# Optimization experiments

Measured on AMD Instinct MI355X. Metric: run time of the kernel, lower is better.

Reference implementation:

```python
import jax, jax.numpy as jnp
import numpy as np

N, D, H, E, K = 4096, 256, 1024, 8, 2  # tokens, hid_dim, expert hidden, n_experts, topk


def setup_inputs() -> dict:
    key = jax.random.key(0)
    ks = jax.random.split(key, 5)
    s = 0.02
    return {
        "x": jax.random.normal(ks[0], (N, D), jnp.float32),
        "gate_W": jax.random.normal(ks[1], (E, D), jnp.float32) * s,  # nn.Linear(hid_dim, n_exp).weight
        "gate_b": jnp.zeros((E,), jnp.float32),
        "W1": jax.random.normal(ks[2], (E, D, H), jnp.float32) * s,   # per-expert FFN layer 1
        "b1": jnp.zeros((E, H), jnp.float32),
        "W2": jax.random.normal(ks[3], (E, H, D), jnp.float32) * s,   # per-expert FFN layer 2
        "b2": jnp.zeros((E, D), jnp.float32),
        "temperature": jnp.array(1.0, jnp.float32),
    }


def reference(x, gate_W, gate_b, W1, b1, W2, b2, temperature):
    # forward() unsqueezes 2D input to [N, 1, D]
    x3 = x[:, None, :]                                           # [N,1,D]
    # _router: gate linear over last dim, squeeze L=1
    gate_scores = (jnp.einsum('nld,ed->nle', x3, gate_W) + gate_b)[:, 0, :]  # [N,E]
    gate_scores = gate_scores / temperature                      # router_act='lambda' -> identity
    _, topk_idx = jax.lax.top_k(gate_scores, K)                  # [N,K]

    # _moe_batch_forward: repeat_interleave tokens K times, route slot s to expert topk_idx.flat[s]
    xs = jnp.repeat(x3, K, axis=0)                               # [N*K,1,D]
    eid = topk_idx.reshape(-1)                                   # [N*K] int
    out = jnp.zeros((N * K, 1, D), x.dtype)
    for e in range(E):  # small fixed expert loop; masks partition the slots
        h = jax.nn.relu(jnp.einsum('sld,dh->slh', xs, W1[e]) + b1[e])  # [N*K,1,H]
        y = jnp.einsum('slh,hd->sld', h, W2[e]) + b2[e]                # [N*K,1,D]
        out = out + jnp.where((eid == e)[:, None, None], y, 0.0)
    out = out.reshape(N, K, 1, D)
    # gatter='sum': sum over the K expert slots -> [N,1,D]
    return out.sum(axis=1)
```

## Files before the change

kernel.cpp:

```cpp
#include <hip/hip_runtime.h>
#include <hip/hip_bf16.h>
#include <stdint.h>

#define NTOK 4096
#define DIM  256
#define HID  1024
#define NEXP 8
#define MTILE 32
#define HC 32
#define HSLICE 512
#define NSLICE 2
#define NCHUNK (HSLICE / HC)

typedef float f32x4 __attribute__((ext_vector_type(4)));
typedef short s16x8 __attribute__((ext_vector_type(8)));

__device__ __forceinline__ unsigned short f2bf(float f) {
  union { float f; unsigned u; } v; v.f = f;
  unsigned r = v.u + 0x7FFFu + ((v.u >> 16) & 1u);
  return (unsigned short)(r >> 16);
}
__device__ __forceinline__ float bf2f(unsigned short s) {
  union { float f; unsigned u; } v; v.u = ((unsigned)s) << 16;
  return v.f;
}
__device__ __forceinline__ void mfma16(f32x4& acc, s16x8 a, s16x8 b) {
  asm("v_mfma_f32_16x16x32_bf16 %0, %1, %2, %0" : "+v"(acc) : "v"(a), "v"(b));
}
__device__ __forceinline__ void accfence(f32x4& a) {
  asm volatile("s_nop 7" : "+v"(a));
}
__device__ __forceinline__ void initfence(f32x4& a) {
  asm volatile("s_nop 1" : "+v"(a));
}

__global__ __launch_bounds__(256) void prep(const float* __restrict__ W1,
                                            const float* __restrict__ W2,
                                            unsigned short* __restrict__ W1T,
                                            unsigned short* __restrict__ W2T,
                                            int* __restrict__ counts) {
  __shared__ float tile[32][33];
  int id = blockIdx.x;
  int tx = threadIdx.x, ty = threadIdx.y;
  if (id == 0 && ty == 0 && tx < NEXP) counts[tx] = 0;

  const float* in; unsigned short* out; int R, C, bx, by, e, sw;
  if (id < 2048) {
    e = id >> 8; int rem = id & 255; by = rem >> 5; bx = rem & 31;
    in = W1; out = W1T; R = 256; C = 1024; sw = 1;
  } else {
    int id2 = id - 2048;
    e = id2 >> 8; int rem = id2 & 255; by = (rem >> 3) & 31; bx = rem & 7;
    in = W2; out = W2T; R = 1024; C = 256; sw = 0;
  }
  int r0 = by * 32, c0 = bx * 32;
  const float* ip = in + (size_t)e * R * C;
  unsigned short* op = out + (size_t)e * R * C;
  #pragma unroll
  for (int k = 0; k < 4; ++k)
    tile[ty + 8*k][tx] = ip[(size_t)(r0 + ty + 8*k) * C + c0 + tx];
  __syncthreads();
  #pragma unroll
  for (int k = 0; k < 4; ++k) {
    float v = tile[tx][ty + 8*k];
    if (sw) {
      int row = c0 + ty + 8*k;
      int col = r0 + tx;
      op[(size_t)row * R + (col ^ ((row & 7) << 3))] = f2bf(v);
    } else {
      int d = c0 + ty + 8*k;
      int h = r0 + tx;
      int ch = h >> 5, kk = h & 31;
      int slot = (kk >> 3) ^ ((d >> 1) & 3);
      op[(size_t)ch * (DIM * 32) + d * 32 + slot * 8 + (kk & 7)] = f2bf(v);
    }
  }
}

__global__ __launch_bounds__(256) void gate_route(const float* __restrict__ x,
    const float* __restrict__ gW, const float* __restrict__ gb,
    const float* __restrict__ temp,
    int* __restrict__ counts, int* __restrict__ list,
    unsigned short* __restrict__ xbf) {
  __shared__ int pairs[16][2];
  __shared__ int lcnt[NEXP], lbase[NEXP], lrank[NEXP];
  int tid = threadIdx.x;
  int w = tid >> 6, lane = tid & 63;
  int sl = lane & 15, g = lane >> 4;
  if (tid < NEXP) { lcnt[tid] = 0; lrank[tid] = 0; }
  __syncthreads();
  int t0 = blockIdx.x * 16;
  int tok = w * 4 + g;
  int n = t0 + tok;

  float4 xv[4];
  #pragma unroll
  for (int p = 0; p < 4; ++p)
    xv[p] = *reinterpret_cast<const float4*>(x + (size_t)n * DIM + sl * 16 + p * 4);
  {
    s16x8 xb0, xb1;
    xb0[0]=(short)f2bf(xv[0].x); xb0[1]=(short)f2bf(xv[0].y); xb0[2]=(short)f2bf(xv[0].z); xb0[3]=(short)f2bf(xv[0].w);
    xb0[4]=(short)f2bf(xv[1].x); xb0[5]=(short)f2bf(xv[1].y); xb0[6]=(short)f2bf(xv[1].z); xb0[7]=(short)f2bf(xv[1].w);
    xb1[0]=(short)f2bf(xv[2].x); xb1[1]=(short)f2bf(xv[2].y); xb1[2]=(short)f2bf(xv[2].z); xb1[3]=(short)f2bf(xv[2].w);
    xb1[4]=(short)f2bf(xv[3].x); xb1[5]=(short)f2bf(xv[3].y); xb1[6]=(short)f2bf(xv[3].z); xb1[7]=(short)f2bf(xv[3].w);
    *reinterpret_cast<s16x8*>(xbf + (size_t)n * DIM + sl * 16)     = xb0;
    *reinterpret_cast<s16x8*>(xbf + (size_t)n * DIM + sl * 16 + 8) = xb1;
  }
  float acc[NEXP];
  #pragma unroll
  for (int e = 0; e < NEXP; ++e) {
    const float* we = gW + (size_t)e * DIM + sl * 16;
    float a = 0.f;
    #pragma unroll
    for (int p = 0; p < 4; ++p) {
      float4 wv = *reinterpret_cast<const float4*>(we + p * 4);
      a += xv[p].x*wv.x + xv[p].y*wv.y + xv[p].z*wv.z + xv[p].w*wv.w;
    }
    acc[e] = a;
  }
  #pragma unroll
  for (int off = 1; off < 16; off <<= 1) {
    #pragma unroll
    for (int e = 0; e < NEXP; ++e) acc[e] += __shfl_xor(acc[e], off);
  }
  if (sl == 0) {
    float t = temp[0];
    float s[NEXP];
    #pragma unroll
    for (int e = 0; e < NEXP; ++e) s[e] = (acc[e] + gb[e]) / t;
    int b0 = 0; float v0 = s[0];
    #pragma unroll
    for (int e = 1; e < NEXP; ++e) if (s[e] > v0) { v0 = s[e]; b0 = e; }
    int b1i = 0; float v1 = -3.4e38f;
    #pragma unroll
    for (int e = 0; e < NEXP; ++e) if (e != b0 && s[e] > v1) { v1 = s[e]; b1i = e; }
    pairs[tok][0] = b0;
    pairs[tok][1] = b1i;
    atomicAdd(&lcnt[b0], 1);
    atomicAdd(&lcnt[b1i], 1);
  }
  __syncthreads();
  if (tid < NEXP) lbase[tid] = atomicAdd(&counts[tid], lcnt[tid]);
  __syncthreads();
  if (tid < 32) {
    int tk = tid >> 1;
    int e = pairs[tk][tid & 1];
    int r = atomicAdd(&lrank[e], 1);
    list[e * NTOK + lbase[e] + r] = (t0 + tk) * 2 + (tid & 1);
  }
}

__global__ __launch_bounds__(256, 2) void moe_ffn(
    const unsigned short* __restrict__ xbf,
    const unsigned short* __restrict__ W1T,
    const unsigned short* __restrict__ W2T,
    const float* __restrict__ b1g, const float* __restrict__ b2g,
    const int* __restrict__ counts, const int* __restrict__ list,
    unsigned short* __restrict__ ybuf) {
  int b = blockIdx.x;
  int e = b & 7;
  int r = b >> 3;
  int s = r & (NSLICE - 1);
  int t = r >> 1;
  int cnt = counts[e];
  if (t * MTILE >= cnt) return;

  __shared__ __align__(16) short W1b[2][HC * 256];
  __shared__ __align__(16) short W2b[2][256 * HC];
  __shared__ __align__(16) short hs[2][32][40];

  int tid = threadIdx.x;
  int l = tid & 63, w = tid >> 6;
  int lr = l & 15, lg = l >> 4, kg = lg * 8;
  int wm = w & 1, wn = w >> 1;
  int hbase = s * HSLICE;
  const int* mylist = list + e * NTOK + t * MTILE;
  const unsigned short* W1e = W1T + (size_t)e * HID * DIM;
  const unsigned short* W2e = W2T + (size_t)e * HID * DIM;

  auto stage1 = [&](int hc, int buf) {
    const char* src = (const char*)(W1e + (size_t)hc * DIM);
    char* dst = (char*)&W1b[buf][0];
    #pragma unroll
    for (int i = 0; i < 4; ++i) {
      int off = w * 4096 + i * 1024;
      __builtin_amdgcn_global_load_lds(
        (const __attribute__((address_space(1))) void*)(src + off + l * 16),
        (__attribute__((address_space(3))) void*)(dst + off), 16, 0, 0);
    }
  };
  auto stage2 = [&](int hc, int buf) {
    const char* src = (const char*)(W2e + (size_t)(hc >> 5) * (DIM * 32));
    char* dst = (char*)&W2b[buf][0];
    #pragma unroll
    for (int i = 0; i < 4; ++i) {
      int off = w * 4096 + i * 1024;
      __builtin_amdgcn_global_load_lds(
        (const __attribute__((address_space(1))) void*)(src + off + l * 16),
        (__attribute__((address_space(3))) void*)(dst + off), 16, 0, 0);
    }
  };

  stage1(hbase, 0);

  float bbreg[NCHUNK];
  #pragma unroll
  for (int c = 0; c < NCHUNK; ++c)
    bbreg[c] = b1g[e * HID + hbase + c * HC + wn * 16 + lr];

  s16x8 xa[8];
  {
    int row = wm * 16 + lr;
    int grow = t * MTILE + row;
    int entry = (grow < cnt) ? mylist[row] : mylist[0];
    const unsigned short* xsrc = xbf + (size_t)(entry >> 1) * DIM;
    #pragma unroll
    for (int kb = 0; kb < 8; ++kb)
      xa[kb] = *(const s16x8*)(xsrc + kb * 32 + kg);
  }

  f32x4 acc[8] = {};
  #pragma unroll
  for (int n = 0; n < 8; ++n) initfence(acc[n]);

  __syncthreads();

  int swz = (lr & 7) << 3;
  int brow = (wn * 16 + lr) << 8;

  #pragma unroll
  for (int c = 0; c < NCHUNK; ++c) {
    int P = c & 1, Q = P ^ 1;

    asm volatile("s_waitcnt lgkmcnt(0)" ::: "memory");
    __builtin_amdgcn_s_barrier();
    __builtin_amdgcn_sched_barrier(0);

    stage1(hbase + (((c + 1) & (NCHUNK - 1)) * HC), Q);
    stage2(hbase + c * HC, P);

    asm volatile("s_waitcnt vmcnt(8)" ::: "memory");
    __builtin_amdgcn_sched_barrier(0);

    f32x4 h0 = {}, h1 = {};
    initfence(h0); initfence(h1);
    const short* w1p = &W1b[P][0];
    #pragma unroll
    for (int kb = 0; kb < 8; ++kb) {
      s16x8 bv = *(const s16x8*)&w1p[brow + ((kb * 32 + kg) ^ swz)];
      if (kb & 1) mfma16(h1, xa[kb], bv); else mfma16(h0, xa[kb], bv);
    }

    if (c > 0) {
      s16x8 a0 = *(const s16x8*)&hs[Q][wm * 16 + lr][kg];
      const short* w2p = &W2b[Q][0];
      #pragma unroll
      for (int n = 0; n < 8; ++n) {
        int d = wn * 128 + n * 16 + lr;
        s16x8 bv = *(const s16x8*)&w2p[(d << 5) + ((lg ^ ((d >> 1) & 3)) << 3)];
        mfma16(acc[n], a0, bv);
      }
    }

    accfence(h0); accfence(h1);
    h0 += h1;
    float bb = bbreg[c];
    #pragma unroll
    for (int q = 0; q < 4; ++q)
      hs[P][wm * 16 + lg * 4 + q][wn * 16 + lr] = (short)f2bf(fmaxf(h0[q] + bb, 0.f));
  }

  asm volatile("s_waitcnt vmcnt(0) lgkmcnt(0)" ::: "memory");
  __builtin_amdgcn_s_barrier();
  __builtin_amdgcn_sched_barrier(0);
  {
    const int Q = (NCHUNK - 1) & 1;
    s16x8 a0 = *(const s16x8*)&hs[Q][wm * 16 + lr][kg];
    const short* w2p = &W2b[Q][0];
    #pragma unroll
    for (int n = 0; n < 8; ++n) {
      int d = wn * 128 + n * 16 + lr;
      s16x8 bv = *(const s16x8*)&w2p[(d << 5) + ((lg ^ ((d >> 1) & 3)) << 3)];
      mfma16(acc[n], a0, bv);
    }
  }

  #pragma unroll
  for (int n = 0; n < 8; ++n) accfence(acc[n]);
  float b2v[8];
  #pragma unroll
  for (int n = 0; n < 8; ++n) b2v[n] = (s == 0) ? b2g[e * DIM + wn * 128 + n * 16 + lr] : 0.f;
  #pragma unroll
  for (int q = 0; q < 4; ++q) {
    int lrow = wm * 16 + lg * 4 + q;
    int grow = t * MTILE + lrow;
    if (grow < cnt) {
      int entry = mylist[lrow];
      unsigned short* yrow = ybuf + ((size_t)entry * NSLICE + s) * DIM + wn * 128 + lr;
      #pragma unroll
      for (int n = 0; n < 8; ++n)
        yrow[n * 16] = f2bf(acc[n][q] + b2v[n]);
    }
  }
}

__global__ __launch_bounds__(256) void reduce4(const unsigned short* __restrict__ yb,
                                               float* __restrict__ out) {
  int i = (blockIdx.x * 256 + threadIdx.x) * 8;
  int n = i >> 8, d = i & 255;
  const unsigned short* base = yb + ((size_t)n * 4) * DIM + d;
  float sum[8] = {0,0,0,0,0,0,0,0};
  #pragma unroll
  for (int r = 0; r < 4; ++r) {
    s16x8 v = *(const s16x8*)(base + r * DIM);
    #pragma unroll
    for (int j = 0; j < 8; ++j) sum[j] += bf2f((unsigned short)v[j]);
  }
  float4 o0 = {sum[0], sum[1], sum[2], sum[3]};
  float4 o1 = {sum[4], sum[5], sum[6], sum[7]};
  *(float4*)(out + i) = o0;
  *(float4*)(out + i + 4) = o1;
}

extern "C" void kernel_launch(void* const* d_in, const int* in_sizes, int n_in,
                              void* d_out, int out_size, void* d_ws, size_t ws_size,
                              hipStream_t stream) {
  const float* x    = (const float*)d_in[0];
  const float* gW   = (const float*)d_in[1];
  const float* gb   = (const float*)d_in[2];
  const float* W1   = (const float*)d_in[3];
  const float* b1   = (const float*)d_in[4];
  const float* W2   = (const float*)d_in[5];
  const float* b2   = (const float*)d_in[6];
  const float* temp = (const float*)d_in[7];
  float* out = (float*)d_out;

  char* ws = (char*)d_ws;
  int*            counts = (int*)(ws + 0);
  int*            list   = (int*)(ws + 256);
  unsigned short* xbf    = (unsigned short*)(ws + 131584);
  unsigned short* W1T    = (unsigned short*)(ws + 2228736);
  unsigned short* W2T    = (unsigned short*)(ws + 6423040);
  unsigned short* ybuf   = (unsigned short*)(ws + 10617344);

  prep<<<4096, dim3(32, 8, 1), 0, stream>>>(W1, W2, W1T, W2T, counts);
  gate_route<<<NTOK/16, 256, 0, stream>>>(x, gW, gb, temp, counts, list, xbf);
  moe_ffn<<<NEXP * (NTOK/MTILE) * NSLICE, 256, 0, stream>>>(xbf, W1T, W2T, b1, b2, counts, list, ybuf);
  reduce4<<<NTOK*DIM/2048, 256, 0, stream>>>(ybuf, out);
}
```

Before: 56.23 us.

## Double token tile per block and split expert hidden dim into four slices

The FFN kernel now handles 64 routed tokens per block instead of 32, with each wave computing two 16-row M fragments. Each W1/W2 fragment read from LDS feeds two MFMAs, so weight staging per token is halved. To keep the grid size unchanged, the hidden dimension is split into four 256-wide slices instead of two. The cost is twice as many bf16 partial outputs written to ybuf, and the final reduce kernel now sums eight partial rows per token instead of four, which adds global memory traffic and accumulator register pressure.

```diff
diff --git a/kernel.cpp b/kernel.cpp
--- a/kernel.cpp
+++ b/kernel.cpp
@@ -6,10 +6,10 @@
 #define DIM  256
 #define HID  1024
 #define NEXP 8
-#define MTILE 32
+#define MTILE 64
 #define HC 32
-#define HSLICE 512
-#define NSLICE 2
+#define HSLICE 256
+#define NSLICE 4
 #define NCHUNK (HSLICE / HC)
 
 typedef float f32x4 __attribute__((ext_vector_type(4)));
@@ -161,13 +161,13 @@
   int e = b & 7;
   int r = b >> 3;
   int s = r & (NSLICE - 1);
-  int t = r >> 1;
+  int t = r >> 2;
   int cnt = counts[e];
   if (t * MTILE >= cnt) return;
 
   __shared__ __align__(16) short W1b[2][HC * 256];
   __shared__ __align__(16) short W2b[2][256 * HC];
-  __shared__ __align__(16) short hs[2][32][40];
+  __shared__ __align__(16) short hs[2][64][40];
 
   int tid = threadIdx.x;
   int l = tid & 63, w = tid >> 6;
@@ -208,20 +208,24 @@
   for (int c = 0; c < NCHUNK; ++c)
     bbreg[c] = b1g[e * HID + hbase + c * HC + wn * 16 + lr];
 
-  s16x8 xa[8];
-  {
-    int row = wm * 16 + lr;
+  s16x8 xa[2][8];
+  #pragma unroll
+  for (int mf = 0; mf < 2; ++mf) {
+    int row = (wm * 2 + mf) * 16 + lr;
     int grow = t * MTILE + row;
     int entry = (grow < cnt) ? mylist[row] : mylist[0];
     const unsigned short* xsrc = xbf + (size_t)(entry >> 1) * DIM;
     #pragma unroll
     for (int kb = 0; kb < 8; ++kb)
-      xa[kb] = *(const s16x8*)(xsrc + kb * 32 + kg);
-  }
-
-  f32x4 acc[8] = {};
-  #pragma unroll
-  for (int n = 0; n < 8; ++n) initfence(acc[n]);
+      xa[mf][kb] = *(const s16x8*)(xsrc + kb * 32 + kg);
+  }
+
+  f32x4 acc[2][8] = {};
+  #pragma unroll
+  for (int mf = 0; mf < 2; ++mf) {
+    #pragma unroll
+    for (int n = 0; n < 8; ++n) initfence(acc[mf][n]);
+  }
 
   __syncthreads();
 
@@ -242,32 +246,38 @@
     asm volatile("s_waitcnt vmcnt(8)" ::: "memory");
     __builtin_amdgcn_sched_barrier(0);
 
-    f32x4 h0 = {}, h1 = {};
-    initfence(h0); initfence(h1);
+    f32x4 h0[2] = {}, h1[2] = {};
+    initfence(h0[0]); initfence(h0[1]); initfence(h1[0]); initfence(h1[1]);
     const short* w1p = &W1b[P][0];
     #pragma unroll
     for (int kb = 0; kb < 8; ++kb) {
       s16x8 bv = *(const s16x8*)&w1p[brow + ((kb * 32 + kg) ^ swz)];
-      if (kb & 1) mfma16(h1, xa[kb], bv); else mfma16(h0, xa[kb], bv);
+      if (kb & 1) { mfma16(h1[0], xa[0][kb], bv); mfma16(h1[1], xa[1][kb], bv); }
+      else        { mfma16(h0[0], xa[0][kb], bv); mfma16(h0[1], xa[1][kb], bv); }
     }
 
     if (c > 0) {
-      s16x8 a0 = *(const s16x8*)&hs[Q][wm * 16 + lr][kg];
+      s16x8 a0 = *(const s16x8*)&hs[Q][(wm * 2 + 0) * 16 + lr][kg];
+      s16x8 a1 = *(const s16x8*)&hs[Q][(wm * 2 + 1) * 16 + lr][kg];
       const short* w2p = &W2b[Q][0];
       #pragma unroll
       for (int n = 0; n < 8; ++n) {
         int d = wn * 128 + n * 16 + lr;
         s16x8 bv = *(const s16x8*)&w2p[(d << 5) + ((lg ^ ((d >> 1) & 3)) << 3)];
-        mfma16(acc[n], a0, bv);
+        mfma16(acc[0][n], a0, bv);
+        mfma16(acc[1][n], a1, bv);
       }
     }
 
-    accfence(h0); accfence(h1);
-    h0 += h1;
+    accfence(h0[0]); accfence(h0[1]); accfence(h1[0]); accfence(h1[1]);
     float bb = bbreg[c];
     #pragma unroll
-    for (int q = 0; q < 4; ++q)
-      hs[P][wm * 16 + lg * 4 + q][wn * 16 + lr] = (short)f2bf(fmaxf(h0[q] + bb, 0.f));
+    for (int mf = 0; mf < 2; ++mf) {
+      f32x4 h = h0[mf] + h1[mf];
+      #pragma unroll
+      for (int q = 0; q < 4; ++q)
+        hs[P][(wm * 2 + mf) * 16 + lg * 4 + q][wn * 16 + lr] = (short)f2bf(fmaxf(h[q] + bb, 0.f));
+    }
   }
 
   asm volatile("s_waitcnt vmcnt(0) lgkmcnt(0)" ::: "memory");
@@ -275,43 +285,51 @@
   __builtin_amdgcn_sched_barrier(0);
   {
     const int Q = (NCHUNK - 1) & 1;
-    s16x8 a0 = *(const s16x8*)&hs[Q][wm * 16 + lr][kg];
+    s16x8 a0 = *(const s16x8*)&hs[Q][(wm * 2 + 0) * 16 + lr][kg];
+    s16x8 a1 = *(const s16x8*)&hs[Q][(wm * 2 + 1) * 16 + lr][kg];
     const short* w2p = &W2b[Q][0];
     #pragma unroll
     for (int n = 0; n < 8; ++n) {
       int d = wn * 128 + n * 16 + lr;
       s16x8 bv = *(const s16x8*)&w2p[(d << 5) + ((lg ^ ((d >> 1) & 3)) << 3)];
-      mfma16(acc[n], a0, bv);
-    }
-  }
-
-  #pragma unroll
-  for (int n = 0; n < 8; ++n) accfence(acc[n]);
+      mfma16(acc[0][n], a0, bv);
+      mfma16(acc[1][n], a1, bv);
+    }
+  }
+
+  #pragma unroll
+  for (int mf = 0; mf < 2; ++mf) {
+    #pragma unroll
+    for (int n = 0; n < 8; ++n) accfence(acc[mf][n]);
+  }
   float b2v[8];
   #pragma unroll
   for (int n = 0; n < 8; ++n) b2v[n] = (s == 0) ? b2g[e * DIM + wn * 128 + n * 16 + lr] : 0.f;
   #pragma unroll
-  for (int q = 0; q < 4; ++q) {
-    int lrow = wm * 16 + lg * 4 + q;
-    int grow = t * MTILE + lrow;
-    if (grow < cnt) {
-      int entry = mylist[lrow];
-      unsigned short* yrow = ybuf + ((size_t)entry * NSLICE + s) * DIM + wn * 128 + lr;
-      #pragma unroll
-      for (int n = 0; n < 8; ++n)
-        yrow[n * 16] = f2bf(acc[n][q] + b2v[n]);
-    }
-  }
-}
-
-__global__ __launch_bounds__(256) void reduce4(const unsigned short* __restrict__ yb,
+  for (int mf = 0; mf < 2; ++mf) {
+    #pragma unroll
+    for (int q = 0; q < 4; ++q) {
+      int lrow = (wm * 2 + mf) * 16 + lg * 4 + q;
+      int grow = t * MTILE + lrow;
+      if (grow < cnt) {
+        int entry = mylist[lrow];
+        unsigned short* yrow = ybuf + ((size_t)entry * NSLICE + s) * DIM + wn * 128 + lr;
+        #pragma unroll
+        for (int n = 0; n < 8; ++n)
+          yrow[n * 16] = f2bf(acc[mf][n][q] + b2v[n]);
+      }
+    }
+  }
+}
+
+__global__ __launch_bounds__(256) void reduce8(const unsigned short* __restrict__ yb,
                                                float* __restrict__ out) {
   int i = (blockIdx.x * 256 + threadIdx.x) * 8;
   int n = i >> 8, d = i & 255;
-  const unsigned short* base = yb + ((size_t)n * 4) * DIM + d;
+  const unsigned short* base = yb + ((size_t)n * 8) * DIM + d;
   float sum[8] = {0,0,0,0,0,0,0,0};
   #pragma unroll
-  for (int r = 0; r < 4; ++r) {
+  for (int r = 0; r < 8; ++r) {
     s16x8 v = *(const s16x8*)(base + r * DIM);
     #pragma unroll
     for (int j = 0; j < 8; ++j) sum[j] += bf2f((unsigned short)v[j]);
@@ -346,5 +364,5 @@
   prep<<<4096, dim3(32, 8, 1), 0, stream>>>(W1, W2, W1T, W2T, counts);
   gate_route<<<NTOK/16, 256, 0, stream>>>(x, gW, gb, temp, counts, list, xbf);
   moe_ffn<<<NEXP * (NTOK/MTILE) * NSLICE, 256, 0, stream>>>(xbf, W1T, W2T, b1, b2, counts, list, ybuf);
-  reduce4<<<NTOK*DIM/2048, 256, 0, stream>>>(ybuf, out);
-}
+  reduce8<<<NTOK*DIM/2048, 256, 0, stream>>>(ybuf, out);
+}
```

New measurement: 52.64 us. 1.07x faster.

## Fuse prep and gating, persist MoE blocks over 64-row tiles with 4 hidden slices

Applied to the files above, without the earlier changes.

Merges the weight transpose/convert kernel and the gate/route kernel into one launch, with the counts reset moved to a memset. The FFN kernel now uses 512-thread blocks covering 64-row tiles, splits the hidden dimension into 4 slices, and has a fixed grid of persistent blocks that loop over tiles with stride 16. The reduction sums 8 partials per token instead of 4. The goals are fewer launches, less idle-block overhead, and more parallelism per expert, at the cost of writing and reading twice the partial-output traffic in bf16. The loop's weight staging and barrier logic is also more fragile.

```diff
diff --git a/kernel.cpp b/kernel.cpp
--- a/kernel.cpp
+++ b/kernel.cpp
@@ -6,10 +6,10 @@
 #define DIM  256
 #define HID  1024
 #define NEXP 8
-#define MTILE 32
+#define MTILE 64
 #define HC 32
-#define HSLICE 512
-#define NSLICE 2
+#define HSLICE 256
+#define NSLICE 4
 #define NCHUNK (HSLICE / HC)
 
 typedef float f32x4 __attribute__((ext_vector_type(4)));
@@ -34,62 +34,60 @@
   asm volatile("s_nop 1" : "+v"(a));
 }
 
-__global__ __launch_bounds__(256) void prep(const float* __restrict__ W1,
-                                            const float* __restrict__ W2,
-                                            unsigned short* __restrict__ W1T,
-                                            unsigned short* __restrict__ W2T,
-                                            int* __restrict__ counts) {
-  __shared__ float tile[32][33];
+__global__ __launch_bounds__(256) void prep_gate(
+    const float* __restrict__ W1, const float* __restrict__ W2,
+    unsigned short* __restrict__ W1T, unsigned short* __restrict__ W2T,
+    const float* __restrict__ x, const float* __restrict__ gW,
+    const float* __restrict__ gb, const float* __restrict__ temp,
+    int* __restrict__ counts, int* __restrict__ list,
+    unsigned short* __restrict__ xbf) {
   int id = blockIdx.x;
   int tx = threadIdx.x, ty = threadIdx.y;
-  if (id == 0 && ty == 0 && tx < NEXP) counts[tx] = 0;
-
-  const float* in; unsigned short* out; int R, C, bx, by, e, sw;
-  if (id < 2048) {
-    e = id >> 8; int rem = id & 255; by = rem >> 5; bx = rem & 31;
-    in = W1; out = W1T; R = 256; C = 1024; sw = 1;
-  } else {
-    int id2 = id - 2048;
-    e = id2 >> 8; int rem = id2 & 255; by = (rem >> 3) & 31; bx = rem & 7;
-    in = W2; out = W2T; R = 1024; C = 256; sw = 0;
-  }
-  int r0 = by * 32, c0 = bx * 32;
-  const float* ip = in + (size_t)e * R * C;
-  unsigned short* op = out + (size_t)e * R * C;
-  #pragma unroll
-  for (int k = 0; k < 4; ++k)
-    tile[ty + 8*k][tx] = ip[(size_t)(r0 + ty + 8*k) * C + c0 + tx];
-  __syncthreads();
-  #pragma unroll
-  for (int k = 0; k < 4; ++k) {
-    float v = tile[tx][ty + 8*k];
-    if (sw) {
-      int row = c0 + ty + 8*k;
-      int col = r0 + tx;
-      op[(size_t)row * R + (col ^ ((row & 7) << 3))] = f2bf(v);
+
+  if (id < 4096) {
+    __shared__ float tile[32][33];
+    const float* in; unsigned short* out; int R, C, bx, by, e, sw;
+    if (id < 2048) {
+      e = id >> 8; int rem = id & 255; by = rem >> 5; bx = rem & 31;
+      in = W1; out = W1T; R = 256; C = 1024; sw = 1;
     } else {
-      int d = c0 + ty + 8*k;
-      int h = r0 + tx;
-      int ch = h >> 5, kk = h & 31;
-      int slot = (kk >> 3) ^ ((d >> 1) & 3);
-      op[(size_t)ch * (DIM * 32) + d * 32 + slot * 8 + (kk & 7)] = f2bf(v);
-    }
-  }
-}
-
-__global__ __launch_bounds__(256) void gate_route(const float* __restrict__ x,
-    const float* __restrict__ gW, const float* __restrict__ gb,
-    const float* __restrict__ temp,
-    int* __restrict__ counts, int* __restrict__ list,
-    unsigned short* __restrict__ xbf) {
+      int id2 = id - 2048;
+      e = id2 >> 8; int rem = id2 & 255; by = (rem >> 3) & 31; bx = rem & 7;
+      in = W2; out = W2T; R = 1024; C = 256; sw = 0;
+    }
+    int r0 = by * 32, c0 = bx * 32;
+    const float* ip = in + (size_t)e * R * C;
+    unsigned short* op = out + (size_t)e * R * C;
+    #pragma unroll
+    for (int k = 0; k < 4; ++k)
+      tile[ty + 8*k][tx] = ip[(size_t)(r0 + ty + 8*k) * C + c0 + tx];
+    __syncthreads();
+    #pragma unroll
+    for (int k = 0; k < 4; ++k) {
+      float v = tile[tx][ty + 8*k];
+      if (sw) {
+        int row = c0 + ty + 8*k;
+        int col = r0 + tx;
+        op[(size_t)row * R + (col ^ ((row & 7) << 3))] = f2bf(v);
+      } else {
+        int d = c0 + ty + 8*k;
+        int h = r0 + tx;
+        int ch = h >> 5, kk = h & 31;
+        int slot = (kk >> 3) ^ ((d >> 1) & 3);
+        op[(size_t)ch * (DIM * 32) + d * 32 + slot * 8 + (kk & 7)] = f2bf(v);
+      }
+    }
+    return;
+  }
+
   __shared__ int pairs[16][2];
   __shared__ int lcnt[NEXP], lbase[NEXP], lrank[NEXP];
-  int tid = threadIdx.x;
+  int tid = ty * 32 + tx;
   int w = tid >> 6, lane = tid & 63;
   int sl = lane & 15, g = lane >> 4;
   if (tid < NEXP) { lcnt[tid] = 0; lrank[tid] = 0; }
   __syncthreads();
-  int t0 = blockIdx.x * 16;
+  int t0 = (id - 4096) * 16;
   int tok = w * 4 + g;
   int n = t0 + tok;
 
@@ -150,7 +148,7 @@
   }
 }
 
-__global__ __launch_bounds__(256, 2) void moe_ffn(
+__global__ __launch_bounds__(512, 4) void moe_ffn(
     const unsigned short* __restrict__ xbf,
     const unsigned short* __restrict__ W1T,
     const unsigned short* __restrict__ W2T,
@@ -161,20 +159,19 @@
   int e = b & 7;
   int r = b >> 3;
   int s = r & (NSLICE - 1);
-  int t = r >> 1;
+  int t = r >> 2;
   int cnt = counts[e];
   if (t * MTILE >= cnt) return;
 
   __shared__ __align__(16) short W1b[2][HC * 256];
   __shared__ __align__(16) short W2b[2][256 * HC];
-  __shared__ __align__(16) short hs[2][32][40];
+  __shared__ __align__(16) short hs[2][64][40];
 
   int tid = threadIdx.x;
   int l = tid & 63, w = tid >> 6;
   int lr = l & 15, lg = l >> 4, kg = lg * 8;
-  int wm = w & 1, wn = w >> 1;
+  int wm = w & 3, wn = w >> 2;
   int hbase = s * HSLICE;
-  const int* mylist = list + e * NTOK + t * MTILE;
   const unsigned short* W1e = W1T + (size_t)e * HID * DIM;
   const unsigned short* W2e = W2T + (size_t)e * HID * DIM;
 
@@ -182,8 +179,8 @@
     const char* src = (const char*)(W1e + (size_t)hc * DIM);
     char* dst = (char*)&W1b[buf][0];
     #pragma unroll
-    for (int i = 0; i < 4; ++i) {
-      int off = w * 4096 + i * 1024;
+    for (int i = 0; i < 2; ++i) {
+      int off = w * 2048 + i * 1024;
       __builtin_amdgcn_global_load_lds(
         (const __attribute__((address_space(1))) void*)(src + off + l * 16),
         (__attribute__((address_space(3))) void*)(dst + off), 16, 0, 0);
@@ -193,65 +190,100 @@
     const char* src = (const char*)(W2e + (size_t)(hc >> 5) * (DIM * 32));
     char* dst = (char*)&W2b[buf][0];
     #pragma unroll
-    for (int i = 0; i < 4; ++i) {
-      int off = w * 4096 + i * 1024;
+    for (int i = 0; i < 2; ++i) {
+      int off = w * 2048 + i * 1024;
       __builtin_amdgcn_global_load_lds(
         (const __attribute__((address_space(1))) void*)(src + off + l * 16),
         (__attribute__((address_space(3))) void*)(dst + off), 16, 0, 0);
     }
   };
 
-  stage1(hbase, 0);
-
   float bbreg[NCHUNK];
   #pragma unroll
   for (int c = 0; c < NCHUNK; ++c)
     bbreg[c] = b1g[e * HID + hbase + c * HC + wn * 16 + lr];
 
-  s16x8 xa[8];
-  {
-    int row = wm * 16 + lr;
-    int grow = t * MTILE + row;
-    int entry = (grow < cnt) ? mylist[row] : mylist[0];
-    const unsigned short* xsrc = xbf + (size_t)(entry >> 1) * DIM;
-    #pragma unroll
-    for (int kb = 0; kb < 8; ++kb)
-      xa[kb] = *(const s16x8*)(xsrc + kb * 32 + kg);
-  }
-
-  f32x4 acc[8] = {};
-  #pragma unroll
-  for (int n = 0; n < 8; ++n) initfence(acc[n]);
-
-  __syncthreads();
+  float b2v[8];
+  #pragma unroll
+  for (int n = 0; n < 8; ++n)
+    b2v[n] = (s == 0) ? b2g[e * DIM + wn * 128 + n * 16 + lr] : 0.f;
 
   int swz = (lr & 7) << 3;
   int brow = (wn * 16 + lr) << 8;
 
-  #pragma unroll
-  for (int c = 0; c < NCHUNK; ++c) {
-    int P = c & 1, Q = P ^ 1;
-
-    asm volatile("s_waitcnt lgkmcnt(0)" ::: "memory");
+  bool first_tile = true;
+  for (int tt = t; tt * MTILE < cnt; tt += 16) {
+    const int* mylist = list + e * NTOK + tt * MTILE;
+
+    if (first_tile) stage1(hbase, 0);
+
+    s16x8 xa[8];
+    {
+      int row = wm * 16 + lr;
+      int grow = tt * MTILE + row;
+      int entry = (grow < cnt) ? mylist[row] : mylist[0];
+      const unsigned short* xsrc = xbf + (size_t)(entry >> 1) * DIM;
+      #pragma unroll
+      for (int kb = 0; kb < 8; ++kb)
+        xa[kb] = *(const s16x8*)(xsrc + kb * 32 + kg);
+    }
+
+    f32x4 acc[8] = {};
+    #pragma unroll
+    for (int n = 0; n < 8; ++n) initfence(acc[n]);
+
+    if (first_tile) {
+      __syncthreads();
+      first_tile = false;
+    }
+
+    #pragma unroll
+    for (int c = 0; c < NCHUNK; ++c) {
+      int P = c & 1, Q = P ^ 1;
+
+      asm volatile("s_waitcnt lgkmcnt(0)" ::: "memory");
+      __builtin_amdgcn_s_barrier();
+      __builtin_amdgcn_sched_barrier(0);
+
+      stage1(hbase + (((c + 1) & (NCHUNK - 1)) * HC), Q);
+      stage2(hbase + c * HC, P);
+
+      asm volatile("s_waitcnt vmcnt(4)" ::: "memory");
+      __builtin_amdgcn_sched_barrier(0);
+
+      f32x4 h0 = {}, h1 = {};
+      initfence(h0); initfence(h1);
+      const short* w1p = &W1b[P][0];
+      #pragma unroll
+      for (int kb = 0; kb < 8; ++kb) {
+        s16x8 bv = *(const s16x8*)&w1p[brow + ((kb * 32 + kg) ^ swz)];
+        if (kb & 1) mfma16(h1, xa[kb], bv); else mfma16(h0, xa[kb], bv);
+      }
+
+      if (c > 0) {
+        s16x8 a0 = *(const s16x8*)&hs[Q][wm * 16 + lr][kg];
+        const short* w2p = &W2b[Q][0];
+        #pragma unroll
+        for (int n = 0; n < 8; ++n) {
+          int d = wn * 128 + n * 16 + lr;
+          s16x8 bv = *(const s16x8*)&w2p[(d << 5) + ((lg ^ ((d >> 1) & 3)) << 3)];
+          mfma16(acc[n], a0, bv);
+        }
+      }
+
+      accfence(h0); accfence(h1);
+      h0 += h1;
+      float bb = bbreg[c];
+      #pragma unroll
+      for (int q = 0; q < 4; ++q)
+        hs[P][wm * 16 + lg * 4 + q][wn * 16 + lr] = (short)f2bf(fmaxf(h0[q] + bb, 0.f));
+    }
+
+    asm volatile("s_waitcnt vmcnt(0) lgkmcnt(0)" ::: "memory");
     __builtin_amdgcn_s_barrier();
     __builtin_amdgcn_sched_barrier(0);
-
-    stage1(hbase + (((c + 1) & (NCHUNK - 1)) * HC), Q);
-    stage2(hbase + c * HC, P);
-
-    asm volatile("s_waitcnt vmcnt(8)" ::: "memory");
-    __builtin_amdgcn_sched_barrier(0);
-
-    f32x4 h0 = {}, h1 = {};
-    initfence(h0); initfence(h1);
-    const short* w1p = &W1b[P][0];
-    #pragma unroll
-    for (int kb = 0; kb < 8; ++kb) {
-      s16x8 bv = *(const s16x8*)&w1p[brow + ((kb * 32 + kg) ^ swz)];
-      if (kb & 1) mfma16(h1, xa[kb], bv); else mfma16(h0, xa[kb], bv);
-    }
-
-    if (c > 0) {
+    {
+      const int Q = (NCHUNK - 1) & 1;
       s16x8 a0 = *(const s16x8*)&hs[Q][wm * 16 + lr][kg];
       const short* w2p = &W2b[Q][0];
       #pragma unroll
@@ -262,56 +294,31 @@
       }
     }
 
-    accfence(h0); accfence(h1);
-    h0 += h1;
-    float bb = bbreg[c];
-    #pragma unroll
-    for (int q = 0; q < 4; ++q)
-      hs[P][wm * 16 + lg * 4 + q][wn * 16 + lr] = (short)f2bf(fmaxf(h0[q] + bb, 0.f));
-  }
-
-  asm volatile("s_waitcnt vmcnt(0) lgkmcnt(0)" ::: "memory");
-  __builtin_amdgcn_s_barrier();
-  __builtin_amdgcn_sched_barrier(0);
-  {
-    const int Q = (NCHUNK - 1) & 1;
-    s16x8 a0 = *(const s16x8*)&hs[Q][wm * 16 + lr][kg];
-    const short* w2p = &W2b[Q][0];
-    #pragma unroll
-    for (int n = 0; n < 8; ++n) {
-      int d = wn * 128 + n * 16 + lr;
-      s16x8 bv = *(const s16x8*)&w2p[(d << 5) + ((lg ^ ((d >> 1) & 3)) << 3)];
-      mfma16(acc[n], a0, bv);
-    }
-  }
-
-  #pragma unroll
-  for (int n = 0; n < 8; ++n) accfence(acc[n]);
-  float b2v[8];
-  #pragma unroll
-  for (int n = 0; n < 8; ++n) b2v[n] = (s == 0) ? b2g[e * DIM + wn * 128 + n * 16 + lr] : 0.f;
-  #pragma unroll
-  for (int q = 0; q < 4; ++q) {
-    int lrow = wm * 16 + lg * 4 + q;
-    int grow = t * MTILE + lrow;
-    if (grow < cnt) {
-      int entry = mylist[lrow];
-      unsigned short* yrow = ybuf + ((size_t)entry * NSLICE + s) * DIM + wn * 128 + lr;
-      #pragma unroll
-      for (int n = 0; n < 8; ++n)
-        yrow[n * 16] = f2bf(acc[n][q] + b2v[n]);
-    }
-  }
-}
-
-__global__ __launch_bounds__(256) void reduce4(const unsigned short* __restrict__ yb,
+    #pragma unroll
+    for (int n = 0; n < 8; ++n) accfence(acc[n]);
+    #pragma unroll
+    for (int q = 0; q < 4; ++q) {
+      int lrow = wm * 16 + lg * 4 + q;
+      int grow = tt * MTILE + lrow;
+      if (grow < cnt) {
+        int entry = mylist[lrow];
+        unsigned short* yrow = ybuf + ((size_t)entry * NSLICE + s) * DIM + wn * 128 + lr;
+        #pragma unroll
+        for (int n = 0; n < 8; ++n)
+          yrow[n * 16] = f2bf(acc[n][q] + b2v[n]);
+      }
+    }
+  }
+}
+
+__global__ __launch_bounds__(256) void reduce8(const unsigned short* __restrict__ yb,
                                                float* __restrict__ out) {
   int i = (blockIdx.x * 256 + threadIdx.x) * 8;
   int n = i >> 8, d = i & 255;
-  const unsigned short* base = yb + ((size_t)n * 4) * DIM + d;
+  const unsigned short* base = yb + ((size_t)n * 8) * DIM + d;
   float sum[8] = {0,0,0,0,0,0,0,0};
   #pragma unroll
-  for (int r = 0; r < 4; ++r) {
+  for (int r = 0; r < 8; ++r) {
     s16x8 v = *(const s16x8*)(base + r * DIM);
     #pragma unroll
     for (int j = 0; j < 8; ++j) sum[j] += bf2f((unsigned short)v[j]);
@@ -343,8 +350,9 @@
   unsigned short* W2T    = (unsigned short*)(ws + 6423040);
   unsigned short* ybuf   = (unsigned short*)(ws + 10617344);
 
-  prep<<<4096, dim3(32, 8, 1), 0, stream>>>(W1, W2, W1T, W2T, counts);
-  gate_route<<<NTOK/16, 256, 0, stream>>>(x, gW, gb, temp, counts, list, xbf);
-  moe_ffn<<<NEXP * (NTOK/MTILE) * NSLICE, 256, 0, stream>>>(xbf, W1T, W2T, b1, b2, counts, list, ybuf);
-  reduce4<<<NTOK*DIM/2048, 256, 0, stream>>>(ybuf, out);
-}
+  hipMemsetAsync(counts, 0, 256, stream);
+  prep_gate<<<4096 + NTOK/16, dim3(32, 8, 1), 0, stream>>>(
+      W1, W2, W1T, W2T, x, gW, gb, temp, counts, list, xbf);
+  moe_ffn<<<NEXP * 16 * NSLICE, 512, 0, stream>>>(xbf, W1T, W2T, b1, b2, counts, list, ybuf);
+  reduce8<<<NTOK*DIM/2048, 256, 0, stream>>>(ybuf, out);
+}
```

New measurement: 70.80 us. +25.9%, slower.
